# Kernel optimization log

Measured on AMD Instinct MI355X. Metric: run time of the kernel, lower is better.

The kernel has to match this reference:

```python
import jax, jax.numpy as jnp
import numpy as np

N, V, C, M, K, D = 20000, 100000, 5000, 32, 2048, 128


def setup_inputs() -> dict:
    key = jax.random.key(0)
    ks = jax.random.split(key, 16)
    inp = {
        "node_emb": jax.random.normal(ks[0], (N, D), jnp.float32),
        "member_score": jax.random.uniform(ks[1], (C, M), jnp.float32),
        "community_embeddings": jax.random.normal(ks[2], (V, D), jnp.float32),
        # MLP params: lins = Linear(3D, D) -> ReLU -> Linear(D, 1)
        "W1": jax.random.normal(ks[3], (3 * D, D), jnp.float32) / np.sqrt(3 * D),
        "b1": jnp.zeros((D,), jnp.float32),
        "W2": jax.random.normal(ks[4], (D, 1), jnp.float32) / np.sqrt(D),
        "b2": jnp.zeros((1,), jnp.float32),
        # lins2 = Linear(D, D//2) -> ReLU -> Linear(D//2, 1)
        "W3": jax.random.normal(ks[5], (D, D // 2), jnp.float32) / np.sqrt(D),
        "b3": jnp.zeros((D // 2,), jnp.float32),
        "W4": jax.random.normal(ks[6], (D // 2, 1), jnp.float32) / np.sqrt(D // 2),
        "b4": jnp.zeros((1,), jnp.float32),
        # integer structure tensors
        "node2community": jax.random.randint(ks[7], (V,), 0, C, jnp.int32),
        "community2node": jax.random.randint(ks[8], (C, M), 0, V, jnp.int32),
        "member_num": jax.random.randint(ks[9], (C,), 0, M, jnp.int32),
        "community_index": jax.random.randint(ks[10], (K,), 0, C, jnp.int32),
        "nodes": jax.random.randint(ks[11], (N,), 0, V, jnp.int32),
    }
    return inp


def reference(node_emb, member_score, community_embeddings, W1, b1, W2, b2, W3, b3, W4, b4,
              node2community, community2node, member_num, community_index, nodes):
    # dense membership table: is community c in community_index?
    in_active = jnp.zeros((C,), jnp.bool_).at[community_index].set(True)  # [C]

    comm = node2community[nodes]              # [N] community of each batch node
    use = in_active[comm]                     # [N] bool: node's community is active
    community_emd = community_embeddings[nodes]  # [N, D]

    members = community2node[comm]            # [N, M] member node ids
    neigh_com = node2community[members]       # [N, M] member communities
    len_mask = jnp.arange(M)[None, :] < member_num[comm][:, None]  # [N, M]
    valid = len_mask & in_active[neigh_com]   # [N, M]

    score = jnp.where(valid, member_score[comm], 0.0)              # [N, M]
    # weighted sum of member-community embeddings (masked entries contribute 0)
    member_embedding = jnp.einsum("nm,nmd->nd", score, community_embeddings[neigh_com])

    feat = jnp.concatenate([node_emb, community_emd, member_embedding], axis=1)  # [N, 3D]
    pred1 = (jax.nn.relu(feat @ W1 + b1) @ W2 + b2)[:, 0]          # active-path score
    pred2 = (jax.nn.relu(node_emb @ W3 + b3) @ W4 + b4)[:, 0]      # inactive-path score
    return jnp.where(use, pred1, pred2)       # [N]


if __name__ == "__main__":
    out = reference(**setup_inputs())
    print(out.shape, out.dtype)
```

## Files before the change

### kernel.cpp

```cpp
#include <hip/hip_runtime.h>

#define NN 20000
#define VV 100000
#define CC 5000
#define MM 32
#define KK 2048
#define DD 128

#define WS_MEMB 32768
#define WS_W1F  2592768
#define WS_W3F  2691072

typedef __attribute__((ext_vector_type(8))) short bf16x8;
typedef __attribute__((ext_vector_type(4))) float f32x4;

__device__ __forceinline__ unsigned f2bf_rne(float f) {
  unsigned u = __builtin_bit_cast(unsigned, f);
  u += 0x7fffu + ((u >> 16) & 1u);
  return u >> 16;
}

__global__ __launch_bounds__(256) void init_k(const int* __restrict__ cidx,
    int* __restrict__ active, const float* __restrict__ W1,
    unsigned short* __restrict__ w1f, const float* __restrict__ W3,
    unsigned short* __restrict__ w3f) {
  int b = blockIdx.x, tid = threadIdx.x;
  if (b == 0) {
    for (int i = tid; i < CC; i += 256) active[i] = 0;
    __syncthreads();
    for (int k = tid; k < KK; k += 256) active[cidx[k]] = 1;
  } else if (b <= 192) {
    int i = (b - 1) * 256 + tid;
    int e = i & 7, slot = i >> 3;
    int lane = slot & 63, g = slot >> 6;
    int ks = g % 12, ct = g / 12;
    int c = ct * 16 + (lane & 15);
    int k = ks * 32 + (lane >> 4) * 8 + e;
    w1f[i] = (unsigned short)f2bf_rne(W1[(size_t)k * DD + c]);
  } else {
    for (int i = tid; i < 64 * DD; i += 256) {
      int e = i & 7, slot = i >> 3;
      int lane = slot & 63, g = slot >> 6;
      int ks = g & 3, ct = g >> 2;
      int h = ct * 16 + (lane & 15);
      int k = ks * 32 + (lane >> 4) * 8 + e;
      w3f[i] = (unsigned short)f2bf_rne(W3[(size_t)k * 64 + h]);
    }
  }
}

__global__ __launch_bounds__(128, 4) void member_emb_k(const int* __restrict__ c2n,
    const int* __restrict__ n2c, const float* __restrict__ mscore,
    const int* __restrict__ mnum, const int* __restrict__ active,
    const int* __restrict__ cidx, const float* __restrict__ cemb,
    float* __restrict__ memb) {
  int c = cidx[blockIdx.x];
  __shared__ float s_sc[MM];
  __shared__ int s_nc[MM];
  int t = threadIdx.x;
  if (t < MM) {
    int mem = c2n[c * MM + t];
    int nc = n2c[mem];
    bool valid = (t < mnum[c]) && (active[nc] != 0);
    s_nc[t] = nc;
    s_sc[t] = valid ? mscore[c * MM + t] : 0.f;
  }
  __syncthreads();
  float a0 = 0.f, a1 = 0.f, a2 = 0.f, a3 = 0.f;
  #pragma unroll
  for (int m = 0; m < MM; m += 4) {
    a0 = fmaf(s_sc[m + 0], cemb[(size_t)s_nc[m + 0] * DD + t], a0);
    a1 = fmaf(s_sc[m + 1], cemb[(size_t)s_nc[m + 1] * DD + t], a1);
    a2 = fmaf(s_sc[m + 2], cemb[(size_t)s_nc[m + 2] * DD + t], a2);
    a3 = fmaf(s_sc[m + 3], cemb[(size_t)s_nc[m + 3] * DD + t], a3);
  }
  memb[(size_t)c * DD + t] = ((a0 + a1) + (a2 + a3));
}

__global__ __launch_bounds__(512, 4) void main_k(const float* __restrict__ node_emb,
    const float* __restrict__ cemb, const float* __restrict__ memb,
    const unsigned short* __restrict__ w1f, const float* __restrict__ b1,
    const float* __restrict__ W2, const float* __restrict__ b2v,
    const unsigned short* __restrict__ w3f, const float* __restrict__ b3,
    const float* __restrict__ W4, const float* __restrict__ b4v,
    const int* __restrict__ n2c, const int* __restrict__ active,
    const int* __restrict__ nodes, float* __restrict__ out) {
  __shared__ __align__(16) unsigned short s_hi[2 * 12 * 64 * 8];
  __shared__ int s_v[32], s_cm[32], s_use[32];
  __shared__ float s_r1[32][8], s_r2[32][4];
  int tid = threadIdx.x;
  int n0 = blockIdx.x * 32;
  if (tid < 32) {
    int v = nodes[n0 + tid], cm = n2c[v];
    s_v[tid] = v; s_cm[tid] = cm; s_use[tid] = active[cm];
  }
  __syncthreads();
  {
    float4 f[6];
    int baseidx[6];
    #pragma unroll
    for (int it = 0; it < 6; ++it) {
      int i4 = it * 512 + tid;
      int row = i4 / 96, pos = i4 % 96;
      int off = pos * 4;
      int use = s_use[row];
      const float* src;
      bool live = true;
      if (off < DD) {
        src = node_emb + (size_t)(n0 + row) * DD + off;
      } else if (off < 2 * DD) {
        src = cemb + (size_t)s_v[row] * DD + (off - DD);
        live = use != 0;
      } else {
        src = memb + (size_t)s_cm[row] * DD + (off - 2 * DD);
        live = use != 0;
      }
      f[it] = live ? *(const float4*)src : make_float4(0.f, 0.f, 0.f, 0.f);
      int rt = row >> 4, r16 = row & 15;
      baseidx[it] = rt * 6144
                  + (((off >> 5) * 64) + r16 + 16 * ((off >> 3) & 3)) * 8 + (off & 7);
    }
    #pragma unroll
    for (int it = 0; it < 6; ++it) {
      unsigned h0 = f2bf_rne(f[it].x), h1 = f2bf_rne(f[it].y),
               h2 = f2bf_rne(f[it].z), h3 = f2bf_rne(f[it].w);
      *(uint2*)&s_hi[baseidx[it]] = make_uint2(h0 | (h1 << 16), h2 | (h3 << 16));
    }
  }
  __syncthreads();
  int lane = tid & 63, w = tid >> 6;
  int lrow = lane & 15, lkq = lane >> 4;
  const bf16x8* ahf = (const bf16x8*)s_hi;
  const bf16x8* b1f = (const bf16x8*)w1f + (size_t)w * 12 * 64 + lane;
  const bf16x8* b3f = (const bf16x8*)w3f + (size_t)(w & 3) * 4 * 64 + lane;
  f32x4 acc[2] = {{0.f, 0.f, 0.f, 0.f}, {0.f, 0.f, 0.f, 0.f}};
  f32x4 p2[2]  = {{0.f, 0.f, 0.f, 0.f}, {0.f, 0.f, 0.f, 0.f}};
  #pragma unroll
  for (int ks = 0; ks < 4; ++ks) {
    bf16x8 va0 = ahf[ks * 64 + lane];
    bf16x8 va1 = ahf[768 + ks * 64 + lane];
    bf16x8 vb0 = b1f[ks * 64];
    bf16x8 vb2 = b3f[ks * 64];
    acc[0] = __builtin_amdgcn_mfma_f32_16x16x32_bf16(va0, vb0, acc[0], 0, 0, 0);
    acc[1] = __builtin_amdgcn_mfma_f32_16x16x32_bf16(va1, vb0, acc[1], 0, 0, 0);
    p2[0]  = __builtin_amdgcn_mfma_f32_16x16x32_bf16(va0, vb2, p2[0], 0, 0, 0);
    p2[1]  = __builtin_amdgcn_mfma_f32_16x16x32_bf16(va1, vb2, p2[1], 0, 0, 0);
  }
  #pragma unroll
  for (int ks = 4; ks < 12; ++ks) {
    bf16x8 va0 = ahf[ks * 64 + lane];
    bf16x8 va1 = ahf[768 + ks * 64 + lane];
    bf16x8 vb0 = b1f[ks * 64];
    acc[0] = __builtin_amdgcn_mfma_f32_16x16x32_bf16(va0, vb0, acc[0], 0, 0, 0);
    acc[1] = __builtin_amdgcn_mfma_f32_16x16x32_bf16(va1, vb0, acc[1], 0, 0, 0);
  }
  {
    int c0 = w * 16 + lrow;
    float b1a = b1[c0], w2a = W2[c0];
    #pragma unroll
    for (int rt = 0; rt < 2; ++rt) {
      float vsum[4];
      #pragma unroll
      for (int j = 0; j < 4; ++j) vsum[j] = fmaxf(acc[rt][j] + b1a, 0.f) * w2a;
      #pragma unroll
      for (int m = 1; m <= 8; m <<= 1)
        #pragma unroll
        for (int j = 0; j < 4; ++j) vsum[j] += __shfl_xor(vsum[j], m, 64);
      if (lrow == 0) {
        #pragma unroll
        for (int j = 0; j < 4; ++j) s_r1[rt * 16 + lkq * 4 + j][w] = vsum[j];
      }
    }
  }
  {
    int h = (w & 3) * 16 + lrow;
    float b3v = b3[h], w4v = W4[h];
    #pragma unroll
    for (int rt = 0; rt < 2; ++rt) {
      float q[4];
      #pragma unroll
      for (int j = 0; j < 4; ++j) q[j] = fmaxf(p2[rt][j] + b3v, 0.f) * w4v;
      #pragma unroll
      for (int m = 1; m <= 8; m <<= 1)
        #pragma unroll
        for (int j = 0; j < 4; ++j) q[j] += __shfl_xor(q[j], m, 64);
      if (lrow == 0 && w < 4) {
        #pragma unroll
        for (int j = 0; j < 4; ++j) s_r2[rt * 16 + lkq * 4 + j][w] = q[j];
      }
    }
  }
  __syncthreads();
  if (tid < 32) {
    float r;
    if (s_use[tid]) {
      r = b2v[0];
      #pragma unroll
      for (int c = 0; c < 8; ++c) r += s_r1[tid][c];
    } else {
      r = s_r2[tid][0] + s_r2[tid][1] + s_r2[tid][2] + s_r2[tid][3] + b4v[0];
    }
    out[n0 + tid] = r;
  }
}

extern "C" void kernel_launch(void* const* d_in, const int* in_sizes, int n_in,
                              void* d_out, int out_size, void* d_ws, size_t ws_size,
                              hipStream_t stream) {
  const float* node_emb = (const float*)d_in[0];
  const float* mscore   = (const float*)d_in[1];
  const float* cemb     = (const float*)d_in[2];
  const float* W1 = (const float*)d_in[3];
  const float* b1 = (const float*)d_in[4];
  const float* W2 = (const float*)d_in[5];
  const float* b2 = (const float*)d_in[6];
  const float* W3 = (const float*)d_in[7];
  const float* b3 = (const float*)d_in[8];
  const float* W4 = (const float*)d_in[9];
  const float* b4 = (const float*)d_in[10];
  const int* n2c   = (const int*)d_in[11];
  const int* c2n   = (const int*)d_in[12];
  const int* mnum  = (const int*)d_in[13];
  const int* cidx  = (const int*)d_in[14];
  const int* nodes = (const int*)d_in[15];
  float* out = (float*)d_out;

  int* active = (int*)d_ws;
  float* memb = (float*)((char*)d_ws + WS_MEMB);
  unsigned short* w1f = (unsigned short*)((char*)d_ws + WS_W1F);
  unsigned short* w3f = (unsigned short*)((char*)d_ws + WS_W3F);

  init_k<<<194, 256, 0, stream>>>(cidx, active, W1, w1f, W3, w3f);
  member_emb_k<<<KK, 128, 0, stream>>>(c2n, n2c, mscore, mnum, active, cidx,
                                       cemb, memb);
  main_k<<<NN / 32, 512, 0, stream>>>(node_emb, cemb, memb, w1f, b1, W2, b2,
                                      w3f, b3, W4, b4, n2c, active, nodes, out);
}
```

Before: 27.09 us.

## Split main kernel block into two 16-row tiles with software-pipelined loads

```diff
diff --git a/kernel.cpp b/kernel.cpp
--- a/kernel.cpp
+++ b/kernel.cpp
@@ -85,123 +85,131 @@
     const float* __restrict__ W4, const float* __restrict__ b4v,
     const int* __restrict__ n2c, const int* __restrict__ active,
     const int* __restrict__ nodes, float* __restrict__ out) {
-  __shared__ __align__(16) unsigned short s_hi[2 * 12 * 64 * 8];
-  __shared__ int s_v[32], s_cm[32], s_use[32];
-  __shared__ float s_r1[32][8], s_r2[32][4];
+  __shared__ __align__(16) unsigned short s_hi[2][6144];
+  __shared__ int s_v[2][16], s_cm[2][16], s_use[2][16];
+  __shared__ float s_r1[2][16][8], s_r2[2][16][4];
   int tid = threadIdx.x;
-  int n0 = blockIdx.x * 32;
-  if (tid < 32) {
-    int v = nodes[n0 + tid], cm = n2c[v];
-    s_v[tid] = v; s_cm[tid] = cm; s_use[tid] = active[cm];
-  }
-  __syncthreads();
-  {
-    float4 f[6];
-    int baseidx[6];
-    #pragma unroll
-    for (int it = 0; it < 6; ++it) {
+  int lane = tid & 63, w = tid >> 6;
+  int lrow = lane & 15, lkq = lane >> 4;
+  int t0 = blockIdx.x * 2, t1 = t0 + 1;
+
+  float4 f[3];
+  int bidx[3];
+
+  auto meta = [&](int bq, int tile) {
+    if (tid < 16) {
+      int v = nodes[tile * 16 + tid], cm = n2c[v];
+      s_v[bq][tid] = v; s_cm[bq][tid] = cm; s_use[bq][tid] = active[cm];
+    }
+  };
+  auto issue = [&](int bq, int tile) {
+    #pragma unroll
+    for (int it = 0; it < 3; ++it) {
       int i4 = it * 512 + tid;
       int row = i4 / 96, pos = i4 % 96;
       int off = pos * 4;
-      int use = s_use[row];
+      int use = s_use[bq][row];
       const float* src;
       bool live = true;
       if (off < DD) {
-        src = node_emb + (size_t)(n0 + row) * DD + off;
+        src = node_emb + (size_t)(tile * 16 + row) * DD + off;
       } else if (off < 2 * DD) {
-        src = cemb + (size_t)s_v[row] * DD + (off - DD);
+        src = cemb + (size_t)s_v[bq][row] * DD + (off - DD);
         live = use != 0;
       } else {
-        src = memb + (size_t)s_cm[row] * DD + (off - 2 * DD);
+        src = memb + (size_t)s_cm[bq][row] * DD + (off - 2 * DD);
         live = use != 0;
       }
       f[it] = live ? *(const float4*)src : make_float4(0.f, 0.f, 0.f, 0.f);
-      int rt = row >> 4, r16 = row & 15;
-      baseidx[it] = rt * 6144
-                  + (((off >> 5) * 64) + r16 + 16 * ((off >> 3) & 3)) * 8 + (off & 7);
-    }
-    #pragma unroll
-    for (int it = 0; it < 6; ++it) {
+      bidx[it] = (((off >> 5) * 64) + row + 16 * ((off >> 3) & 3)) * 8 + (off & 7);
+    }
+  };
+  auto stage_write = [&](int bq) {
+    #pragma unroll
+    for (int it = 0; it < 3; ++it) {
       unsigned h0 = f2bf_rne(f[it].x), h1 = f2bf_rne(f[it].y),
                h2 = f2bf_rne(f[it].z), h3 = f2bf_rne(f[it].w);
-      *(uint2*)&s_hi[baseidx[it]] = make_uint2(h0 | (h1 << 16), h2 | (h3 << 16));
-    }
-  }
-  __syncthreads();
-  int lane = tid & 63, w = tid >> 6;
-  int lrow = lane & 15, lkq = lane >> 4;
-  const bf16x8* ahf = (const bf16x8*)s_hi;
-  const bf16x8* b1f = (const bf16x8*)w1f + (size_t)w * 12 * 64 + lane;
-  const bf16x8* b3f = (const bf16x8*)w3f + (size_t)(w & 3) * 4 * 64 + lane;
-  f32x4 acc[2] = {{0.f, 0.f, 0.f, 0.f}, {0.f, 0.f, 0.f, 0.f}};
-  f32x4 p2[2]  = {{0.f, 0.f, 0.f, 0.f}, {0.f, 0.f, 0.f, 0.f}};
-  #pragma unroll
-  for (int ks = 0; ks < 4; ++ks) {
-    bf16x8 va0 = ahf[ks * 64 + lane];
-    bf16x8 va1 = ahf[768 + ks * 64 + lane];
-    bf16x8 vb0 = b1f[ks * 64];
-    bf16x8 vb2 = b3f[ks * 64];
-    acc[0] = __builtin_amdgcn_mfma_f32_16x16x32_bf16(va0, vb0, acc[0], 0, 0, 0);
-    acc[1] = __builtin_amdgcn_mfma_f32_16x16x32_bf16(va1, vb0, acc[1], 0, 0, 0);
-    p2[0]  = __builtin_amdgcn_mfma_f32_16x16x32_bf16(va0, vb2, p2[0], 0, 0, 0);
-    p2[1]  = __builtin_amdgcn_mfma_f32_16x16x32_bf16(va1, vb2, p2[1], 0, 0, 0);
-  }
-  #pragma unroll
-  for (int ks = 4; ks < 12; ++ks) {
-    bf16x8 va0 = ahf[ks * 64 + lane];
-    bf16x8 va1 = ahf[768 + ks * 64 + lane];
-    bf16x8 vb0 = b1f[ks * 64];
-    acc[0] = __builtin_amdgcn_mfma_f32_16x16x32_bf16(va0, vb0, acc[0], 0, 0, 0);
-    acc[1] = __builtin_amdgcn_mfma_f32_16x16x32_bf16(va1, vb0, acc[1], 0, 0, 0);
-  }
-  {
-    int c0 = w * 16 + lrow;
-    float b1a = b1[c0], w2a = W2[c0];
-    #pragma unroll
-    for (int rt = 0; rt < 2; ++rt) {
+      *(uint2*)&s_hi[bq][bidx[it]] = make_uint2(h0 | (h1 << 16), h2 | (h3 << 16));
+    }
+  };
+  auto compute = [&](int bq) {
+    const bf16x8* ahf = (const bf16x8*)s_hi[bq];
+    const bf16x8* b1f = (const bf16x8*)w1f + (size_t)w * 12 * 64 + lane;
+    const bf16x8* b3f = (const bf16x8*)w3f + (size_t)(w & 3) * 4 * 64 + lane;
+    f32x4 acc = {0.f, 0.f, 0.f, 0.f};
+    f32x4 p2  = {0.f, 0.f, 0.f, 0.f};
+    #pragma unroll
+    for (int ks = 0; ks < 4; ++ks) {
+      bf16x8 va = ahf[ks * 64 + lane];
+      acc = __builtin_amdgcn_mfma_f32_16x16x32_bf16(va, b1f[ks * 64], acc, 0, 0, 0);
+      p2  = __builtin_amdgcn_mfma_f32_16x16x32_bf16(va, b3f[ks * 64], p2, 0, 0, 0);
+    }
+    #pragma unroll
+    for (int ks = 4; ks < 12; ++ks) {
+      bf16x8 va = ahf[ks * 64 + lane];
+      acc = __builtin_amdgcn_mfma_f32_16x16x32_bf16(va, b1f[ks * 64], acc, 0, 0, 0);
+    }
+    {
+      int c0 = w * 16 + lrow;
+      float b1a = b1[c0], w2a = W2[c0];
       float vsum[4];
       #pragma unroll
-      for (int j = 0; j < 4; ++j) vsum[j] = fmaxf(acc[rt][j] + b1a, 0.f) * w2a;
+      for (int j = 0; j < 4; ++j) vsum[j] = fmaxf(acc[j] + b1a, 0.f) * w2a;
       #pragma unroll
       for (int m = 1; m <= 8; m <<= 1)
         #pragma unroll
         for (int j = 0; j < 4; ++j) vsum[j] += __shfl_xor(vsum[j], m, 64);
       if (lrow == 0) {
         #pragma unroll
-        for (int j = 0; j < 4; ++j) s_r1[rt * 16 + lkq * 4 + j][w] = vsum[j];
-      }
-    }
-  }
-  {
-    int h = (w & 3) * 16 + lrow;
-    float b3v = b3[h], w4v = W4[h];
-    #pragma unroll
-    for (int rt = 0; rt < 2; ++rt) {
-      float q[4];
-      #pragma unroll
-      for (int j = 0; j < 4; ++j) q[j] = fmaxf(p2[rt][j] + b3v, 0.f) * w4v;
+        for (int j = 0; j < 4; ++j) s_r1[bq][lkq * 4 + j][w] = vsum[j];
+      }
+    }
+    {
+      int h = (w & 3) * 16 + lrow;
+      float b3v = b3[h], w4v = W4[h];
+      float qq[4];
+      #pragma unroll
+      for (int j = 0; j < 4; ++j) qq[j] = fmaxf(p2[j] + b3v, 0.f) * w4v;
       #pragma unroll
       for (int m = 1; m <= 8; m <<= 1)
         #pragma unroll
-        for (int j = 0; j < 4; ++j) q[j] += __shfl_xor(q[j], m, 64);
+        for (int j = 0; j < 4; ++j) qq[j] += __shfl_xor(qq[j], m, 64);
       if (lrow == 0 && w < 4) {
         #pragma unroll
-        for (int j = 0; j < 4; ++j) s_r2[rt * 16 + lkq * 4 + j][w] = q[j];
-      }
-    }
-  }
-  __syncthreads();
-  if (tid < 32) {
-    float r;
-    if (s_use[tid]) {
-      r = b2v[0];
-      #pragma unroll
-      for (int c = 0; c < 8; ++c) r += s_r1[tid][c];
-    } else {
-      r = s_r2[tid][0] + s_r2[tid][1] + s_r2[tid][2] + s_r2[tid][3] + b4v[0];
-    }
-    out[n0 + tid] = r;
-  }
+        for (int j = 0; j < 4; ++j) s_r2[bq][lkq * 4 + j][w] = qq[j];
+      }
+    }
+  };
+  auto write_out = [&](int bq, int tile) {
+    if (tid < 16) {
+      float r;
+      if (s_use[bq][tid]) {
+        r = b2v[0];
+        #pragma unroll
+        for (int c = 0; c < 8; ++c) r += s_r1[bq][tid][c];
+      } else {
+        r = s_r2[bq][tid][0] + s_r2[bq][tid][1] + s_r2[bq][tid][2]
+          + s_r2[bq][tid][3] + b4v[0];
+      }
+      out[tile * 16 + tid] = r;
+    }
+  };
+
+  meta(0, t0);
+  __syncthreads();
+  issue(0, t0);
+  stage_write(0);
+  meta(1, t1);
+  __syncthreads();
+  issue(1, t1);
+  compute(0);
+  __syncthreads();
+  write_out(0, t0);
+  stage_write(1);
+  __syncthreads();
+  compute(1);
+  __syncthreads();
+  write_out(1, t1);
 }
 
 extern "C" void kernel_launch(void* const* d_in, const int* in_sizes, int n_in,
```

Result: slower. 31.08 us (+14.7%).
